# Performance work log

Measured on AMD Instinct MI355X. Metric: run time of the kernel, lower is better.

## Reference

```python
import jax, jax.numpy as jnp
import numpy as np

B, Q, C, NH, DH = 16, 300, 256, 8, 32
SPATIAL = [(80, 80), (40, 40), (20, 20), (10, 10)]
NPTS = [4, 4, 4, 4]
SUMP = sum(NPTS)
OFFSET_SCALE = 0.5


def _grid_bias():
    # directional init from build(): unit directions per head, scaled 1..n per level
    thetas = np.arange(NH) * (2.0 * np.pi / NH)
    g = np.stack([np.cos(thetas), np.sin(thetas)], -1)
    g = g / np.abs(g).max(-1, keepdims=True)
    g = np.tile(g[:, None, :], (1, SUMP, 1))
    scal = np.concatenate([np.arange(1, n + 1) for n in NPTS])[None, :, None]
    return (g * scal).astype(np.float32)


def setup_inputs() -> dict:
    key = jax.random.key(0)
    ks = jax.random.split(key, 5)
    S = sum(h * w for h, w in SPATIAL)
    return {
        "hidden_states": jax.random.normal(ks[0], (B, Q, C), jnp.float32),
        "encoder_hidden_states": jax.random.normal(ks[1], (B, S, C), jnp.float32),
        "reference_points": jax.random.uniform(ks[2], (B, Q, 1, 4), jnp.float32),
        "off_kernel": jax.random.normal(ks[3], (C, NH, SUMP, 2), jnp.float32) * 0.01,
        "off_bias": jnp.asarray(_grid_bias()),
        "attn_kernel": jax.random.normal(ks[4], (C, NH, SUMP), jnp.float32) * 0.01,
        "attn_bias": jnp.zeros((NH, SUMP), jnp.float32),
        "num_points_scale": jnp.asarray(
            np.concatenate([np.full(n, 1.0 / n) for n in NPTS]).astype(np.float32)
        ),
        "spatial_shapes": jnp.asarray(SPATIAL, jnp.int32),
    }


def _bilinear(v, loc, H, W):
    # v: [B, NH, H*W, DH]; loc: [B, Q, NH, P, 2] normalized in [0,1]
    # grid_sample(bilinear, align_corners=False, zeros padding) on grid 2*loc-1
    x = loc[..., 0] * W - 0.5
    y = loc[..., 1] * H - 0.5
    x0 = jnp.floor(x)
    y0 = jnp.floor(y)
    lx = x - x0
    ly = y - y0
    x0i = x0.astype(jnp.int32)
    y0i = y0.astype(jnp.int32)
    Bv = v.shape[0]
    Ql, Pl = loc.shape[1], loc.shape[3]
    out = jnp.zeros((Bv, NH, Ql, Pl, DH), v.dtype)
    corners = ((0, 0, (1 - lx) * (1 - ly)), (1, 0, lx * (1 - ly)),
               (0, 1, (1 - lx) * ly), (1, 1, lx * ly))
    for dx, dy, w in corners:
        xc = x0i + dx
        yc = y0i + dy
        valid = (xc >= 0) & (xc < W) & (yc >= 0) & (yc < H)
        idx = jnp.clip(yc, 0, H - 1) * W + jnp.clip(xc, 0, W - 1)  # [B,Q,NH,P]
        idx_t = jnp.transpose(idx, (0, 2, 1, 3)).reshape(Bv, NH, Ql * Pl, 1)
        g = jnp.take_along_axis(v, idx_t, axis=2).reshape(Bv, NH, Ql, Pl, DH)
        wt = (w * valid).astype(v.dtype)  # [B,Q,NH,P]
        out = out + g * jnp.transpose(wt, (0, 2, 1, 3))[..., None]
    return out  # [B,NH,Q,P,DH]


def reference(hidden_states, encoder_hidden_states, reference_points, off_kernel,
              off_bias, attn_kernel, attn_bias, num_points_scale, spatial_shapes):
    # sampling offsets / attention weights projections (EinsumDense equivalents)
    offsets = jnp.einsum('bqc,chpt->bqhpt', hidden_states, off_kernel) + off_bias
    attn = jax.nn.softmax(
        jnp.einsum('bqc,chp->bqhp', hidden_states, attn_kernel) + attn_bias, axis=-1)
    # 4-d reference points branch: center + scaled offsets * box wh
    center = jnp.expand_dims(reference_points[..., :2], -2)   # [B,Q,1,1,2]
    wh = jnp.expand_dims(reference_points[..., 2:], -2)       # [B,Q,1,1,2]
    loc = center + offsets * num_points_scale[:, None] * wh * OFFSET_SCALE  # [B,Q,NH,SUMP,2]
    S = encoder_hidden_states.shape[1]
    value = encoder_hidden_states.reshape(B, S, NH, DH).transpose(0, 2, 1, 3)  # [B,NH,S,DH]
    out = jnp.zeros((B, Q, NH, DH), hidden_states.dtype)
    start, pstart = 0, 0
    for (H, W), P in zip(SPATIAL, NPTS):
        v = value[:, :, start:start + H * W, :]
        l = loc[:, :, :, pstart:pstart + P, :]
        sampled = _bilinear(v, l, H, W)  # [B,NH,Q,P,DH]
        out = out + jnp.einsum('bhqpd,bqhp->bqhd', sampled,
                               attn[:, :, :, pstart:pstart + P])
        start += H * W
        pstart += P
    return out.reshape(B, Q, C), attn
```

## Files before the change

kernel.cpp:

```cpp
#include <hip/hip_runtime.h>
#include <math.h>

#define BB 16
#define QQ 300
#define CC 256
#define NHH 8
#define DHH 32
#define SUMPP 16
#define SSS 8500
#define GQ 10
#define QT (QQ / GQ)

__global__ __launch_bounds__(384) void precompute_kernel(
    const float* __restrict__ hs,
    const float* __restrict__ refp,
    const float* __restrict__ off_k,
    const float* __restrict__ off_b,
    const float* __restrict__ attn_k,
    const float* __restrict__ attn_b,
    const float* __restrict__ nps,
    float* __restrict__ loc_out,
    float* __restrict__ attn_out)
{
    const int t = threadIdx.x;
    const int blk = blockIdx.x;
    const int b = blk / QT;
    const int q0 = (blk % QT) * GQ;
    const float* hsb = hs + ((size_t)b * QQ + q0) * CC;

    float acc[GQ];
#pragma unroll
    for (int g = 0; g < GQ; ++g) acc[g] = 0.f;

    if (t < 256) {
        const float* kcol = off_k + t;
#pragma unroll 4
        for (int c = 0; c < CC; ++c) {
            const float k = kcol[c * 256];
#pragma unroll
            for (int g = 0; g < GQ; ++g)
                acc[g] = fmaf(hsb[g * CC + c], k, acc[g]);
        }
        const int p = (t >> 1) & 15;
        const float scale = nps[p] * 0.5f;
        const float bias = off_b[t];
        const bool isy = (t & 1);
#pragma unroll
        for (int g = 0; g < GQ; ++g) {
            const float4 r = *(const float4*)(refp + ((size_t)b * QQ + q0 + g) * 4);
            const float center = isy ? r.y : r.x;
            const float wh     = isy ? r.w : r.z;
            loc_out[((size_t)b * QQ + q0 + g) * 256 + t] =
                fmaf((acc[g] + bias) * scale, wh, center);
        }
    } else {
        const int j = t - 256;
        const float* kcol = attn_k + j;
#pragma unroll 4
        for (int c = 0; c < CC; ++c) {
            const float k = kcol[c * 128];
#pragma unroll
            for (int g = 0; g < GQ; ++g)
                acc[g] = fmaf(hsb[g * CC + c], k, acc[g]);
        }
        const float bias = attn_b[j];
#pragma unroll
        for (int g = 0; g < GQ; ++g) {
            const float logit = acc[g] + bias;
            float m = logit;
#pragma unroll
            for (int o = 1; o < 16; o <<= 1)
                m = fmaxf(m, __shfl_xor(m, o));
            const float e = __expf(logit - m);
            float s = e;
#pragma unroll
            for (int o = 1; o < 16; o <<= 1)
                s += __shfl_xor(s, o);
            attn_out[((size_t)b * QQ + q0 + g) * 128 + j] = e / s;
        }
    }
}

__global__ __launch_bounds__(256) void sample_kernel(
    const float* __restrict__ enc,
    const float* __restrict__ loc,
    const float* __restrict__ attn,
    float* __restrict__ out)
{
    __shared__ float sh_lx[4 * SUMPP * NHH];
    __shared__ float sh_ly[4 * SUMPP * NHH];
    __shared__ float sh_a[4 * SUMPP * NHH];

    const int t = threadIdx.x;
    const int blk = blockIdx.x;
    const int b = blk / (QQ / 4);
    const int q0 = (blk % (QQ / 4)) * 4;
    const size_t qbase = (size_t)b * QQ + q0;

#pragma unroll
    for (int k = 0; k < 4; ++k) {
        const int i = t + k * 256;
        const float v = loc[qbase * 256 + i];
        const int q_i = i >> 8;
        const int r = i & 255;
        const int h_i = r >> 5;
        const int rem = r & 31;
        const int p_i = rem >> 1;
        if (rem & 1) sh_ly[q_i * 128 + p_i * 8 + h_i] = v;
        else         sh_lx[q_i * 128 + p_i * 8 + h_i] = v;
    }
#pragma unroll
    for (int k = 0; k < 2; ++k) {
        const int i = t + k * 256;
        const float v = attn[qbase * 128 + i];
        const int q_i = i >> 7;
        const int r = i & 127;
        const int h_i = r >> 4;
        const int p_i = r & 15;
        sh_a[q_i * 128 + p_i * 8 + h_i] = v;
    }
    __syncthreads();

    const int qs = t >> 6;
    const int lane = t & 63;
    const int h = lane >> 3;
    const int d4 = (lane & 7) << 2;
    const float* vb = enc + (size_t)b * SSS * 256 + h * 32 + d4;

    float4 acc = {0.f, 0.f, 0.f, 0.f};

    const int   HWs[4]    = {80, 40, 20, 10};
    const int   starts[4] = {0, 6400, 8000, 8400};

    int p = 0;
#pragma unroll
    for (int lvl = 0; lvl < 4; ++lvl) {
        const int Wd = HWs[lvl];
        const float Wf = (float)Wd;
        const int st = starts[lvl];
#pragma unroll
        for (int pp = 0; pp < 4; ++pp, ++p) {
            const float locx = sh_lx[qs * 128 + p * 8 + h];
            const float locy = sh_ly[qs * 128 + p * 8 + h];
            const float aw   = sh_a [qs * 128 + p * 8 + h];

            const float x = locx * Wf - 0.5f;
            const float y = locy * Wf - 0.5f;
            const float x0f = floorf(x), y0f = floorf(y);
            const float lx = x - x0f, ly = y - y0f;
            const int x0 = (int)x0f, y0 = (int)y0f;
            const int x1 = x0 + 1, y1 = y0 + 1;
            const float w00 = (1.f - lx) * (1.f - ly);
            const float w10 = lx * (1.f - ly);
            const float w01 = (1.f - lx) * ly;
            const float w11 = lx * ly;
            const bool vx0 = (x0 >= 0) & (x0 < Wd);
            const bool vx1 = (x1 >= 0) & (x1 < Wd);
            const bool vy0 = (y0 >= 0) & (y0 < Wd);
            const bool vy1 = (y1 >= 0) & (y1 < Wd);

            float4 s = {0.f, 0.f, 0.f, 0.f};
            if (vy0) {
                const float* row = vb + (size_t)(st + y0 * Wd) * 256;
                if (vx0) {
                    const float4 v = *(const float4*)(row + (size_t)x0 * 256);
                    s.x += w00 * v.x; s.y += w00 * v.y; s.z += w00 * v.z; s.w += w00 * v.w;
                }
                if (vx1) {
                    const float4 v = *(const float4*)(row + (size_t)x1 * 256);
                    s.x += w10 * v.x; s.y += w10 * v.y; s.z += w10 * v.z; s.w += w10 * v.w;
                }
            }
            if (vy1) {
                const float* row = vb + (size_t)(st + y1 * Wd) * 256;
                if (vx0) {
                    const float4 v = *(const float4*)(row + (size_t)x0 * 256);
                    s.x += w01 * v.x; s.y += w01 * v.y; s.z += w01 * v.z; s.w += w01 * v.w;
                }
                if (vx1) {
                    const float4 v = *(const float4*)(row + (size_t)x1 * 256);
                    s.x += w11 * v.x; s.y += w11 * v.y; s.z += w11 * v.z; s.w += w11 * v.w;
                }
            }
            acc.x += s.x * aw; acc.y += s.y * aw; acc.z += s.z * aw; acc.w += s.w * aw;
        }
    }

    float* op = out + (qbase + qs) * 256 + h * 32 + d4;
    *(float4*)op = acc;
}

extern "C" void kernel_launch(void* const* d_in, const int* in_sizes, int n_in,
                              void* d_out, int out_size, void* d_ws, size_t ws_size,
                              hipStream_t stream) {
    const float* hs     = (const float*)d_in[0];
    const float* enc    = (const float*)d_in[1];
    const float* refp   = (const float*)d_in[2];
    const float* off_k  = (const float*)d_in[3];
    const float* off_b  = (const float*)d_in[4];
    const float* attn_k = (const float*)d_in[5];
    const float* attn_b = (const float*)d_in[6];
    const float* nps    = (const float*)d_in[7];

    float* out      = (float*)d_out;
    float* attn_out = out + (size_t)BB * QQ * NHH * SUMPP * 0 + (size_t)BB * QQ * CC;
    float* loc_ws   = (float*)d_ws;

    precompute_kernel<<<BB * QT, 384, 0, stream>>>(hs, refp, off_k, off_b,
                                                   attn_k, attn_b, nps,
                                                   loc_ws, attn_out);
    sample_kernel<<<BB * (QQ / 4), 256, 0, stream>>>(enc, loc_ws, attn_out, out);
}
```

Before: 279.8 us.

## Pre-transpose loc/attn layouts, branchless clamped bilinear gathers, XCD-aware block mapping

Measured after the change: 244.4 us. 1.14x faster.

```diff
diff --git a/kernel.cpp b/kernel.cpp
--- a/kernel.cpp
+++ b/kernel.cpp
@@ -19,7 +19,8 @@
     const float* __restrict__ attn_k,
     const float* __restrict__ attn_b,
     const float* __restrict__ nps,
-    float* __restrict__ loc_out,
+    float* __restrict__ loc_t,
+    float* __restrict__ aw_t,
     float* __restrict__ attn_out)
 {
     const int t = threadIdx.x;
@@ -33,30 +34,34 @@
     for (int g = 0; g < GQ; ++g) acc[g] = 0.f;
 
     if (t < 256) {
+        const int h = t >> 5;
+        const int p = (t >> 1) & 15;
+        const int xy = t & 1;
         const float* kcol = off_k + t;
-#pragma unroll 4
+#pragma unroll 8
         for (int c = 0; c < CC; ++c) {
             const float k = kcol[c * 256];
 #pragma unroll
             for (int g = 0; g < GQ; ++g)
                 acc[g] = fmaf(hsb[g * CC + c], k, acc[g]);
         }
-        const int p = (t >> 1) & 15;
         const float scale = nps[p] * 0.5f;
         const float bias = off_b[t];
-        const bool isy = (t & 1);
+        const int didx = ((p * 8 + h) << 1) | xy;
 #pragma unroll
         for (int g = 0; g < GQ; ++g) {
             const float4 r = *(const float4*)(refp + ((size_t)b * QQ + q0 + g) * 4);
-            const float center = isy ? r.y : r.x;
-            const float wh     = isy ? r.w : r.z;
-            loc_out[((size_t)b * QQ + q0 + g) * 256 + t] =
+            const float center = xy ? r.y : r.x;
+            const float wh     = xy ? r.w : r.z;
+            loc_t[((size_t)b * QQ + q0 + g) * 256 + didx] =
                 fmaf((acc[g] + bias) * scale, wh, center);
         }
     } else {
         const int j = t - 256;
+        const int h = j >> 4;
+        const int p = j & 15;
         const float* kcol = attn_k + j;
-#pragma unroll 4
+#pragma unroll 8
         for (int c = 0; c < CC; ++c) {
             const float k = kcol[c * 128];
 #pragma unroll
@@ -76,49 +81,36 @@
 #pragma unroll
             for (int o = 1; o < 16; o <<= 1)
                 s += __shfl_xor(s, o);
-            attn_out[((size_t)b * QQ + q0 + g) * 128 + j] = e / s;
+            const float a = e / s;
+            attn_out[((size_t)b * QQ + q0 + g) * 128 + j] = a;
+            aw_t[((size_t)b * QQ + q0 + g) * 128 + p * 8 + h] = a;
         }
     }
 }
 
 __global__ __launch_bounds__(256) void sample_kernel(
     const float* __restrict__ enc,
-    const float* __restrict__ loc,
-    const float* __restrict__ attn,
+    const float2* __restrict__ loc2,
+    const float* __restrict__ aw_t,
     float* __restrict__ out)
 {
-    __shared__ float sh_lx[4 * SUMPP * NHH];
-    __shared__ float sh_ly[4 * SUMPP * NHH];
-    __shared__ float sh_a[4 * SUMPP * NHH];
+    __shared__ float2 sh_l[4 * 128];
+    __shared__ float  sh_a[4 * 128];
+
+    const int g = blockIdx.x;
+    const int xcd = g & 7;
+    const int i = g >> 3;
+    const int b = ((i & 1) << 3) | xcd;
+    const int q0 = (i >> 1) * 4;
+    const size_t qbase = (size_t)b * QQ + q0;
 
     const int t = threadIdx.x;
-    const int blk = blockIdx.x;
-    const int b = blk / (QQ / 4);
-    const int q0 = (blk % (QQ / 4)) * 4;
-    const size_t qbase = (size_t)b * QQ + q0;
-
-#pragma unroll
-    for (int k = 0; k < 4; ++k) {
-        const int i = t + k * 256;
-        const float v = loc[qbase * 256 + i];
-        const int q_i = i >> 8;
-        const int r = i & 255;
-        const int h_i = r >> 5;
-        const int rem = r & 31;
-        const int p_i = rem >> 1;
-        if (rem & 1) sh_ly[q_i * 128 + p_i * 8 + h_i] = v;
-        else         sh_lx[q_i * 128 + p_i * 8 + h_i] = v;
-    }
-#pragma unroll
-    for (int k = 0; k < 2; ++k) {
-        const int i = t + k * 256;
-        const float v = attn[qbase * 128 + i];
-        const int q_i = i >> 7;
-        const int r = i & 127;
-        const int h_i = r >> 4;
-        const int p_i = r & 15;
-        sh_a[q_i * 128 + p_i * 8 + h_i] = v;
-    }
+    const float2* lsrc = loc2 + qbase * 128;
+    sh_l[t] = lsrc[t];
+    sh_l[t + 256] = lsrc[t + 256];
+    const float* asrc = aw_t + qbase * 128;
+    sh_a[t] = asrc[t];
+    sh_a[t + 256] = asrc[t + 256];
     __syncthreads();
 
     const int qs = t >> 6;
@@ -129,8 +121,8 @@
 
     float4 acc = {0.f, 0.f, 0.f, 0.f};
 
-    const int   HWs[4]    = {80, 40, 20, 10};
-    const int   starts[4] = {0, 6400, 8000, 8400};
+    const int HWs[4]    = {80, 40, 20, 10};
+    const int starts[4] = {0, 6400, 8000, 8400};
 
     int p = 0;
 #pragma unroll
@@ -140,49 +132,46 @@
         const int st = starts[lvl];
 #pragma unroll
         for (int pp = 0; pp < 4; ++pp, ++p) {
-            const float locx = sh_lx[qs * 128 + p * 8 + h];
-            const float locy = sh_ly[qs * 128 + p * 8 + h];
-            const float aw   = sh_a [qs * 128 + p * 8 + h];
-
-            const float x = locx * Wf - 0.5f;
-            const float y = locy * Wf - 0.5f;
+            const float2 l = sh_l[qs * 128 + p * 8 + h];
+            const float  a = sh_a[qs * 128 + p * 8 + h];
+
+            const float x = l.x * Wf - 0.5f;
+            const float y = l.y * Wf - 0.5f;
             const float x0f = floorf(x), y0f = floorf(y);
             const float lx = x - x0f, ly = y - y0f;
             const int x0 = (int)x0f, y0 = (int)y0f;
             const int x1 = x0 + 1, y1 = y0 + 1;
-            const float w00 = (1.f - lx) * (1.f - ly);
-            const float w10 = lx * (1.f - ly);
-            const float w01 = (1.f - lx) * ly;
-            const float w11 = lx * ly;
-            const bool vx0 = (x0 >= 0) & (x0 < Wd);
-            const bool vx1 = (x1 >= 0) & (x1 < Wd);
-            const bool vy0 = (y0 >= 0) & (y0 < Wd);
-            const bool vy1 = (y1 >= 0) & (y1 < Wd);
-
-            float4 s = {0.f, 0.f, 0.f, 0.f};
-            if (vy0) {
-                const float* row = vb + (size_t)(st + y0 * Wd) * 256;
-                if (vx0) {
-                    const float4 v = *(const float4*)(row + (size_t)x0 * 256);
-                    s.x += w00 * v.x; s.y += w00 * v.y; s.z += w00 * v.z; s.w += w00 * v.w;
-                }
-                if (vx1) {
-                    const float4 v = *(const float4*)(row + (size_t)x1 * 256);
-                    s.x += w10 * v.x; s.y += w10 * v.y; s.z += w10 * v.z; s.w += w10 * v.w;
-                }
-            }
-            if (vy1) {
-                const float* row = vb + (size_t)(st + y1 * Wd) * 256;
-                if (vx0) {
-                    const float4 v = *(const float4*)(row + (size_t)x0 * 256);
-                    s.x += w01 * v.x; s.y += w01 * v.y; s.z += w01 * v.z; s.w += w01 * v.w;
-                }
-                if (vx1) {
-                    const float4 v = *(const float4*)(row + (size_t)x1 * 256);
-                    s.x += w11 * v.x; s.y += w11 * v.y; s.z += w11 * v.z; s.w += w11 * v.w;
-                }
-            }
-            acc.x += s.x * aw; acc.y += s.y * aw; acc.z += s.z * aw; acc.w += s.w * aw;
+
+            const bool vx0 = (unsigned)x0 < (unsigned)Wd;
+            const bool vx1 = (unsigned)x1 < (unsigned)Wd;
+            const bool vy0 = (unsigned)y0 < (unsigned)Wd;
+            const bool vy1 = (unsigned)y1 < (unsigned)Wd;
+
+            const int x0c = min(max(x0, 0), Wd - 1);
+            const int x1c = min(max(x1, 0), Wd - 1);
+            const int y0c = min(max(y0, 0), Wd - 1);
+            const int y1c = min(max(y1, 0), Wd - 1);
+
+            float w00 = (1.f - lx) * (1.f - ly) * a;
+            float w10 = lx * (1.f - ly) * a;
+            float w01 = (1.f - lx) * ly * a;
+            float w11 = lx * ly * a;
+            w00 = (vx0 & vy0) ? w00 : 0.f;
+            w10 = (vx1 & vy0) ? w10 : 0.f;
+            w01 = (vx0 & vy1) ? w01 : 0.f;
+            w11 = (vx1 & vy1) ? w11 : 0.f;
+
+            const float* r0 = vb + (size_t)(st + y0c * Wd) * 256;
+            const float* r1 = vb + (size_t)(st + y1c * Wd) * 256;
+            const float4 v00 = *(const float4*)(r0 + ((size_t)x0c << 8));
+            const float4 v10 = *(const float4*)(r0 + ((size_t)x1c << 8));
+            const float4 v01 = *(const float4*)(r1 + ((size_t)x0c << 8));
+            const float4 v11 = *(const float4*)(r1 + ((size_t)x1c << 8));
+
+            acc.x = fmaf(w00, v00.x, fmaf(w10, v10.x, fmaf(w01, v01.x, fmaf(w11, v11.x, acc.x))));
+            acc.y = fmaf(w00, v00.y, fmaf(w10, v10.y, fmaf(w01, v01.y, fmaf(w11, v11.y, acc.y))));
+            acc.z = fmaf(w00, v00.z, fmaf(w10, v10.z, fmaf(w01, v01.z, fmaf(w11, v11.z, acc.z))));
+            acc.w = fmaf(w00, v00.w, fmaf(w10, v10.w, fmaf(w01, v01.w, fmaf(w11, v11.w, acc.w))));
         }
     }
 
@@ -203,11 +192,13 @@
     const float* nps    = (const float*)d_in[7];
 
     float* out      = (float*)d_out;
-    float* attn_out = out + (size_t)BB * QQ * NHH * SUMPP * 0 + (size_t)BB * QQ * CC;
-    float* loc_ws   = (float*)d_ws;
+    float* attn_out = out + (size_t)BB * QQ * CC;
+    float* loc_t    = (float*)d_ws;
+    float* aw_t     = loc_t + (size_t)BB * QQ * 256;
 
     precompute_kernel<<<BB * QT, 384, 0, stream>>>(hs, refp, off_k, off_b,
                                                    attn_k, attn_b, nps,
-                                                   loc_ws, attn_out);
-    sample_kernel<<<BB * (QQ / 4), 256, 0, stream>>>(enc, loc_ws, attn_out, out);
+                                                   loc_t, aw_t, attn_out);
+    sample_kernel<<<BB * (QQ / 4), 256, 0, stream>>>(enc, (const float2*)loc_t,
+                                                     aw_t, out);
 }
```
